# Kernel optimization log

Measured on AMD Instinct MI355X. Metric: run time of the kernel, lower is better.

## Reference

```python
import jax, jax.numpy as jnp
import numpy as np

N_A = 50000   # 'user' nodes
N_B = 50000   # 'item' nodes
E = 1000000   # edges per relation
IN, HID, OUT = 128, 128, 64


def setup_inputs() -> dict:
    key = jax.random.key(0)
    ks = jax.random.split(key, 24)
    def glorot(k, shape):
        scale = 1.0 / np.sqrt(shape[0])
        return jax.random.normal(k, shape, jnp.float32) * scale
    inp = {
        "feat_A": jax.random.normal(ks[0], (N_A, IN), jnp.float32),
        "feat_B": jax.random.normal(ks[1], (N_B, IN), jnp.float32),
        "rates_src": jax.random.randint(ks[2], (E,), 0, N_A, jnp.int32),
        "rates_dst": jax.random.randint(ks[3], (E,), 0, N_B, jnp.int32),
        "ratedby_src": jax.random.randint(ks[4], (E,), 0, N_B, jnp.int32),
        "ratedby_dst": jax.random.randint(ks[5], (E,), 0, N_A, jnp.int32),
        "follows_src": jax.random.randint(ks[6], (E,), 0, N_A, jnp.int32),
        "follows_dst": jax.random.randint(ks[7], (E,), 0, N_A, jnp.int32),
        "neg_src": jax.random.randint(ks[8], (E,), 0, N_A, jnp.int32),
        "neg_dst": jax.random.randint(ks[9], (E,), 0, N_B, jnp.int32),
        "W1_rates": glorot(ks[10], (IN, HID)),   "b1_rates": jnp.zeros((HID,), jnp.float32),
        "W1_ratedby": glorot(ks[11], (IN, HID)), "b1_ratedby": jnp.zeros((HID,), jnp.float32),
        "W1_follows": glorot(ks[12], (IN, HID)), "b1_follows": jnp.zeros((HID,), jnp.float32),
        "W2_rates": glorot(ks[13], (HID, OUT)),   "b2_rates": jnp.zeros((OUT,), jnp.float32),
        "W2_ratedby": glorot(ks[14], (HID, OUT)), "b2_ratedby": jnp.zeros((OUT,), jnp.float32),
        "W2_follows": glorot(ks[15], (HID, OUT)), "b2_follows": jnp.zeros((OUT,), jnp.float32),
    }
    return inp


def _graph_conv(x_src, W, b, src, dst, n_src, n_dst):
    # DGL GraphConv, norm='both': D_dst^{-1/2} A D_src^{-1/2} (X W) + b
    ones = jnp.ones(src.shape[0], x_src.dtype)
    deg_out = jnp.maximum(jax.ops.segment_sum(ones, src, num_segments=n_src), 1.0)
    deg_in = jnp.maximum(jax.ops.segment_sum(ones, dst, num_segments=n_dst), 1.0)
    h = (x_src * (deg_out ** -0.5)[:, None]) @ W          # [n_src, d_out]
    agg = jax.ops.segment_sum(h[src], dst, num_segments=n_dst)  # SpMM
    return agg * (deg_in ** -0.5)[:, None] + b


def reference(feat_A, feat_B,
              W1_rates, b1_rates, W1_ratedby, b1_ratedby, W1_follows, b1_follows,
              W2_rates, b2_rates, W2_ratedby, b2_ratedby, W2_follows, b2_follows,
              rates_src, rates_dst, ratedby_src, ratedby_dst,
              follows_src, follows_dst, neg_src, neg_dst):
    # --- RGCN layer 1 (HeteroGraphConv, aggregate='sum') ---
    hB = _graph_conv(feat_A, W1_rates, b1_rates, rates_src, rates_dst, N_A, N_B)
    hA = (_graph_conv(feat_B, W1_ratedby, b1_ratedby, ratedby_src, ratedby_dst, N_B, N_A)
          + _graph_conv(feat_A, W1_follows, b1_follows, follows_src, follows_dst, N_A, N_A))
    hA = jax.nn.relu(hA)
    hB = jax.nn.relu(hB)
    # --- RGCN layer 2 ---
    oB = _graph_conv(hA, W2_rates, b2_rates, rates_src, rates_dst, N_A, N_B)
    oA = (_graph_conv(hB, W2_ratedby, b2_ratedby, ratedby_src, ratedby_dst, N_B, N_A)
          + _graph_conv(hA, W2_follows, b2_follows, follows_src, follows_dst, N_A, N_A))
    # --- HeteroInnerProduct (u_dot_v on etype 'rates') for pos and neg graphs ---
    pos_score = jnp.sum(oA[rates_src] * oB[rates_dst], axis=1, keepdims=True)  # [E, 1]
    neg_score = jnp.sum(oA[neg_src] * oB[neg_dst], axis=1, keepdims=True)      # [E, 1]
    return pos_score, neg_score
```

## Files before the change

### kernel.cpp

```cpp
#include <hip/hip_runtime.h>
#include <hip/hip_fp16.h>
#include <cstddef>
#include <type_traits>

#define N_NODES 50000
#define E_EDGES 1000000
#define NBUCK 196
#define ACHUNK 3907
#define MTILES 3125
#define HB 96
#define HCHUNK 10417
#define GB1 384
#define GB2 256

typedef _Float16 f16x8 __attribute__((ext_vector_type(8)));
typedef float f32x4 __attribute__((ext_vector_type(4)));

__global__ __launch_bounds__(256) void fused0(
        const float* __restrict__ w0, const float* __restrict__ w1,
        const float* __restrict__ w2, const float* __restrict__ w3,
        const float* __restrict__ w4, const float* __restrict__ w5,
        __half* __restrict__ Wt,
        const int* __restrict__ rs, const int* __restrict__ rd,
        const int* __restrict__ bs, const int* __restrict__ bd,
        const int* __restrict__ fs, const int* __restrict__ fd,
        int* __restrict__ bphist) {
    int bx = blockIdx.x;
    if (bx < 6 * HB) {
        __shared__ int l[NBUCK];
        int arr = bx / HB, blk = bx % HB;
        const int* idx = arr == 0 ? rs : arr == 1 ? rd : arr == 2 ? bs
                       : arr == 3 ? bd : arr == 4 ? fs : fd;
        for (int b = threadIdx.x; b < NBUCK; b += 256) l[b] = 0;
        __syncthreads();
        int e0 = blk * HCHUNK;
        int e1 = e0 + HCHUNK; if (e1 > E_EDGES) e1 = E_EDGES;
        for (int i = e0 + threadIdx.x; i < e1; i += 256)
            atomicAdd(&l[((unsigned)idx[i]) >> 8], 1);
        __syncthreads();
        int* dst = bphist + (size_t)(arr * HB + blk) * NBUCK;
        for (int b = threadIdx.x; b < NBUCK; b += 256) dst[b] = l[b];
        return;
    }
    bx -= 6 * HB;
    int m = bx / 16, part = bx % 16;
    const float* W = m == 0 ? w0 : m == 1 ? w1 : m == 2 ? w2 : m == 3 ? w3 : m == 4 ? w4 : w5;
    __half* Tt = Wt + (m < 3 ? m * 16384 : 49152 + (m - 3) * 8192);
    int ncol = m < 3 ? 128 : 64;
    int tot = 128 * ncol;
    for (int i = part * 256 + threadIdx.x; i < tot; i += 16 * 256) {
        int n = i >> 7, k = i & 127;
        Tt[i] = __float2half(W[k * ncol + n]);
    }
}

__global__ void bucket_scan_par(const int* __restrict__ bphist, int* __restrict__ gbase,
                                int* __restrict__ gcur) {
    int arr = blockIdx.x;
    int t = threadIdx.x;
    int c = 0;
    if (t < NBUCK) {
        const int* p = bphist + (size_t)arr * HB * NBUCK + t;
#pragma unroll 8
        for (int blk = 0; blk < HB; blk++) c += p[(size_t)blk * NBUCK];
    }
    int lane = t & 63, wid = t >> 6;
    __shared__ int wsum[4];
    int v = c;
#pragma unroll
    for (int o = 1; o < 64; o <<= 1) { int u = __shfl_up(v, o); if (lane >= o) v += u; }
    if (lane == 63) wsum[wid] = v;
    __syncthreads();
    int base = 0;
    for (int ww = 0; ww < wid; ww++) base += wsum[ww];
    int excl = base + v - c;
    if (t < NBUCK) {
        gbase[arr * (NBUCK + 1) + t] = excl;
        gcur[arr * NBUCK + t] = excl;
    }
    if (t == 255) gbase[arr * (NBUCK + 1) + NBUCK] = base + v;
}

__global__ __launch_bounds__(256) void fused_bin(
        const int* __restrict__ rs, const int* __restrict__ rd,
        const int* __restrict__ bs, const int* __restrict__ bd,
        const int* __restrict__ fs, const int* __restrict__ fd,
        int* __restrict__ gcur, unsigned* __restrict__ pairs,
        unsigned char* __restrict__ sbytes) {
    int y = blockIdx.y;
    __shared__ int lcnt[NBUCK];
    __shared__ int lbase[NBUCK];
    int e0 = blockIdx.x * ACHUNK;
    int e1 = e0 + ACHUNK; if (e1 > E_EDGES) e1 = E_EDGES;
    for (int b = threadIdx.x; b < NBUCK; b += 256) lcnt[b] = 0;
    __syncthreads();
    if (y < 3) {
        int rel = y, arr = 2 * rel + 1;
        const int* src = rel == 0 ? rs : rel == 1 ? bs : fs;
        const int* dst = rel == 0 ? rd : rel == 1 ? bd : fd;
        for (int i = e0 + threadIdx.x; i < e1; i += 256)
            atomicAdd(&lcnt[((unsigned)dst[i]) >> 8], 1);
        __syncthreads();
        for (int b = threadIdx.x; b < NBUCK; b += 256) {
            lbase[b] = lcnt[b] ? atomicAdd(&gcur[arr * NBUCK + b], lcnt[b]) : 0;
            lcnt[b] = 0;
        }
        __syncthreads();
        unsigned* pp = pairs + (size_t)rel * E_EDGES;
        for (int i = e0 + threadIdx.x; i < e1; i += 256) {
            int d = dst[i];
            int b = ((unsigned)d) >> 8;
            int p = lbase[b] + atomicAdd(&lcnt[b], 1);
            pp[p] = ((unsigned)(d & 255) << 16) | (unsigned)src[i];
        }
    } else {
        int rel = y - 3, arr = 2 * rel;
        const int* src = rel == 0 ? rs : rel == 1 ? bs : fs;
        for (int i = e0 + threadIdx.x; i < e1; i += 256)
            atomicAdd(&lcnt[((unsigned)src[i]) >> 8], 1);
        __syncthreads();
        for (int b = threadIdx.x; b < NBUCK; b += 256) {
            lbase[b] = lcnt[b] ? atomicAdd(&gcur[arr * NBUCK + b], lcnt[b]) : 0;
            lcnt[b] = 0;
        }
        __syncthreads();
        unsigned char* sb = sbytes + (size_t)rel * E_EDGES;
        for (int i = e0 + threadIdx.x; i < e1; i += 256) {
            int s = src[i];
            int b = ((unsigned)s) >> 8;
            int p = lbase[b] + atomicAdd(&lcnt[b], 1);
            sb[p] = (unsigned char)(s & 255);
        }
    }
}

__global__ __launch_bounds__(256) void fused_finish(
        const unsigned* __restrict__ pairs, const unsigned char* __restrict__ sbytes,
        const int* __restrict__ gbase, int* __restrict__ row_ptr,
        float* __restrict__ scales, int* __restrict__ col) {
    int y = blockIdx.y, b = blockIdx.x, t = threadIdx.x;
    __shared__ int cnt[256];
    __shared__ int rowbase[256];
    __shared__ int wsum[4];
    if (y < 3) {
        int rel = y, arr = 2 * rel;
        int p0 = gbase[arr * (NBUCK + 1) + b];
        int p1 = gbase[arr * (NBUCK + 1) + b + 1];
        const unsigned char* sb = sbytes + (size_t)rel * E_EDGES;
        cnt[t] = 0;
        __syncthreads();
        for (int i = p0 + t; i < p1; i += 256)
            atomicAdd(&cnt[sb[i]], 1);
        __syncthreads();
        int node = b * 256 + t;
        if (node < N_NODES) {
            int c = cnt[t]; if (c < 1) c = 1;
            scales[(size_t)arr * N_NODES + node] = 1.0f / sqrtf((float)c);
        }
    } else {
        int rel = y - 3, arr = 2 * rel + 1;
        int gb = gbase[arr * (NBUCK + 1) + b];
        int ge = gbase[arr * (NBUCK + 1) + b + 1];
        const unsigned* pp = pairs + (size_t)rel * E_EDGES;
        cnt[t] = 0;
        __syncthreads();
        for (int i = gb + t; i < ge; i += 256)
            atomicAdd(&cnt[pp[i] >> 16], 1);
        __syncthreads();
        int lane = t & 63, wid = t >> 6;
        int c0 = cnt[t];
        int v = c0;
#pragma unroll
        for (int o = 1; o < 64; o <<= 1) { int u = __shfl_up(v, o); if (lane >= o) v += u; }
        if (lane == 63) wsum[wid] = v;
        __syncthreads();
        int base = gb;
        for (int w = 0; w < wid; w++) base += wsum[w];
        int excl = base + v - c0;
        rowbase[t] = excl;
        int node = b * 256 + t;
        if (node <= N_NODES)
            row_ptr[(size_t)rel * (N_NODES + 1) + node] = excl;
        if (node < N_NODES) {
            int c = c0; if (c < 1) c = 1;
            scales[(size_t)arr * N_NODES + node] = 1.0f / sqrtf((float)c);
        }
        cnt[t] = 0;
        __syncthreads();
        int* cl = col + (size_t)rel * E_EDGES;
        for (int i = gb + t; i < ge; i += 256) {
            unsigned p = pp[i];
            int dl = p >> 16;
            int slot = rowbase[dl] + atomicAdd(&cnt[dl], 1);
            cl[slot] = (int)(p & 0xFFFFu);
        }
    }
}

template <int NCOL, typename XT>
__device__ __forceinline__ void gemm_body(const XT* __restrict__ X,
                                          const float* __restrict__ sc,
                                          const __half* __restrict__ Wt,
                                          __half* __restrict__ T,
                                          int bxr, int nblocks) {
    constexpr int NHALF = NCOL / 64;
    int gw = bxr * 4 + ((int)threadIdx.x >> 6);
    int lane = threadIdx.x & 63;
    int half_id = gw % NHALF;
    int mstream = gw / NHALF;
    int nstreams = nblocks * 4 / NHALF;
    int l15 = lane & 15, g = lane >> 4;

    f16x8 b[4][4];
    {
        const __half* wb = Wt + ((size_t)half_id * 64 + l15) * 128 + g * 8;
#pragma unroll
        for (int nt = 0; nt < 4; nt++)
#pragma unroll
            for (int kb = 0; kb < 4; kb++)
                b[nt][kb] = *(const f16x8*)(wb + nt * 16 * 128 + kb * 32);
    }

    for (int mt = mstream; mt < MTILES; mt += nstreams) {
        int m0 = mt * 16;
        f16x8 a[4];
        if constexpr (std::is_same<XT, float>::value) {
            const float* xr = X + (size_t)(m0 + l15) * 128 + g * 8;
#pragma unroll
            for (int kb = 0; kb < 4; kb++) {
                float4 u = *(const float4*)(xr + kb * 32);
                float4 v = *(const float4*)(xr + kb * 32 + 4);
                f16x8 t;
                t[0] = (_Float16)u.x; t[1] = (_Float16)u.y;
                t[2] = (_Float16)u.z; t[3] = (_Float16)u.w;
                t[4] = (_Float16)v.x; t[5] = (_Float16)v.y;
                t[6] = (_Float16)v.z; t[7] = (_Float16)v.w;
                a[kb] = t;
            }
        } else {
            const _Float16* xr = (const _Float16*)X + (size_t)(m0 + l15) * 128 + g * 8;
#pragma unroll
            for (int kb = 0; kb < 4; kb++)
                a[kb] = *(const f16x8*)(xr + kb * 32);
        }
        f32x4 acc[4];
#pragma unroll
        for (int nt = 0; nt < 4; nt++) acc[nt] = (f32x4){0.f, 0.f, 0.f, 0.f};
#pragma unroll
        for (int kb = 0; kb < 4; kb++)
#pragma unroll
            for (int nt = 0; nt < 4; nt++)
                acc[nt] = __builtin_amdgcn_mfma_f32_16x16x32_f16(a[kb], b[nt][kb], acc[nt], 0, 0, 0);
        int mrow = m0 + g * 4;
#pragma unroll
        for (int j = 0; j < 4; j++) {
            float sj = sc[mrow + j];
            __half* tj = T + (size_t)(mrow + j) * NCOL + half_id * 64 + l15;
            tj[0]  = __float2half(acc[0][j] * sj);
            tj[16] = __float2half(acc[1][j] * sj);
            tj[32] = __float2half(acc[2][j] * sj);
            tj[48] = __float2half(acc[3][j] * sj);
        }
    }
}

__global__ __launch_bounds__(256) void gemm_l1(const float* __restrict__ fA,
                                               const float* __restrict__ fB,
                                               const float* __restrict__ scales,
                                               const __half* __restrict__ Wt,
                                               __half* __restrict__ T012) {
    int rel = blockIdx.x / GB1, bxr = blockIdx.x % GB1;
    const float* X = (rel == 1) ? fB : fA;
    const float* sc = scales + (rel == 0 ? 0 : rel == 1 ? 2 * N_NODES : 4 * N_NODES);
    const __half* W = Wt + rel * 16384;
    __half* T = T012 + (size_t)rel * N_NODES * 128;
    gemm_body<128, float>(X, sc, W, T, bxr, GB1);
}

__global__ __launch_bounds__(256) void gemm_l2(const __half* __restrict__ hA,
                                               const __half* __restrict__ hB,
                                               const float* __restrict__ scales,
                                               const __half* __restrict__ Wt,
                                               __half* __restrict__ Tp) {
    int rel = blockIdx.x / GB2, bxr = blockIdx.x % GB2;
    const __half* X = (rel == 1) ? hB : hA;
    const float* sc = scales + (rel == 0 ? 0 : rel == 1 ? 2 * N_NODES : 4 * N_NODES);
    const __half* W = Wt + 49152 + rel * 8192;
    __half* T = Tp + (size_t)rel * N_NODES * 64;
    gemm_body<64, __half>(X, sc, W, T, bxr, GB2);
}

__global__ __launch_bounds__(256) void spmm_l1(
        const int* __restrict__ row_ptr, const int* __restrict__ col,
        const __half* __restrict__ T012, const float* __restrict__ scales,
        const float* __restrict__ b1r, const float* __restrict__ b1rb,
        const float* __restrict__ b1f,
        __half* __restrict__ hB, __half* __restrict__ hA) {
    int w = (blockIdx.x * blockDim.x + threadIdx.x) >> 6;
    int lane = threadIdx.x & 63;
    unsigned loff = (unsigned)lane << 2;
    const char* T0 = (const char*)T012;
    const char* T1 = T0 + (size_t)N_NODES * 256;
    const char* T2 = T1 + (size_t)N_NODES * 256;
#define LDT(B, c) __half22float2(*(const __half2*)((B) + (((unsigned)(c) << 8) + loff)))
    if (w < N_NODES / 2) {
        const int* cl = col;
        int rowA = w * 2, rowB = rowA + 1;
        int eA = row_ptr[rowA], EA = row_ptr[rowA + 1];
        int eB = EA, EB = row_ptr[rowB + 1];
        float axA = 0.f, ayA = 0.f, axB = 0.f, ayB = 0.f;
        while (eA + 4 <= EA && eB + 4 <= EB) {
            int a0 = cl[eA], a1 = cl[eA+1], a2 = cl[eA+2], a3 = cl[eA+3];
            int b0 = cl[eB], b1 = cl[eB+1], b2 = cl[eB+2], b3 = cl[eB+3];
            float2 v0 = LDT(T0, a0), v1 = LDT(T0, a1), v2 = LDT(T0, a2), v3 = LDT(T0, a3);
            float2 u0 = LDT(T0, b0), u1 = LDT(T0, b1), u2 = LDT(T0, b2), u3 = LDT(T0, b3);
            axA += (v0.x + v1.x) + (v2.x + v3.x); ayA += (v0.y + v1.y) + (v2.y + v3.y);
            axB += (u0.x + u1.x) + (u2.x + u3.x); ayB += (u0.y + u1.y) + (u2.y + u3.y);
            eA += 4; eB += 4;
        }
        while (eA + 4 <= EA) {
            int a0 = cl[eA], a1 = cl[eA+1], a2 = cl[eA+2], a3 = cl[eA+3];
            float2 v0 = LDT(T0, a0), v1 = LDT(T0, a1), v2 = LDT(T0, a2), v3 = LDT(T0, a3);
            axA += (v0.x + v1.x) + (v2.x + v3.x); ayA += (v0.y + v1.y) + (v2.y + v3.y);
            eA += 4;
        }
        while (eB + 4 <= EB) {
            int b0 = cl[eB], b1 = cl[eB+1], b2 = cl[eB+2], b3 = cl[eB+3];
            float2 u0 = LDT(T0, b0), u1 = LDT(T0, b1), u2 = LDT(T0, b2), u3 = LDT(T0, b3);
            axB += (u0.x + u1.x) + (u2.x + u3.x); ayB += (u0.y + u1.y) + (u2.y + u3.y);
            eB += 4;
        }
        while (eA < EA && eB < EB) {
            float2 v = LDT(T0, cl[eA]), u = LDT(T0, cl[eB]);
            axA += v.x; ayA += v.y; axB += u.x; ayB += u.y;
            eA++; eB++;
        }
        for (; eA < EA; eA++) { float2 v = LDT(T0, cl[eA]); axA += v.x; ayA += v.y; }
        for (; eB < EB; eB++) { float2 v = LDT(T0, cl[eB]); axB += v.x; ayB += v.y; }
        float bx = b1r[2 * lane], by = b1r[2 * lane + 1];
        float sA = scales[N_NODES + rowA], sB = scales[N_NODES + rowB];
        float ox = fmaxf(fmaf(axA, sA, bx), 0.f), oy = fmaxf(fmaf(ayA, sA, by), 0.f);
        *(__half2*)(hB + (size_t)rowA * 128 + 2 * lane) = __floats2half2_rn(ox, oy);
        ox = fmaxf(fmaf(axB, sB, bx), 0.f); oy = fmaxf(fmaf(ayB, sB, by), 0.f);
        *(__half2*)(hB + (size_t)rowB * 128 + 2 * lane) = __floats2half2_rn(ox, oy);
    } else {
        int r = w - N_NODES / 2;
        const int* rp1 = row_ptr + (N_NODES + 1);
        const int* rp2 = row_ptr + 2 * (N_NODES + 1);
        const int* cl1 = col + E_EDGES;
        const int* cl2 = col + 2 * (size_t)E_EDGES;
        int e1 = rp1[r], E1 = rp1[r + 1];
        int e2 = rp2[r], E2 = rp2[r + 1];
        float a1x = 0.f, a1y = 0.f, a2x = 0.f, a2y = 0.f;
        while (e1 + 4 <= E1 && e2 + 4 <= E2) {
            int a0 = cl1[e1], a1 = cl1[e1+1], a2 = cl1[e1+2], a3 = cl1[e1+3];
            int b0 = cl2[e2], b1 = cl2[e2+1], b2 = cl2[e2+2], b3 = cl2[e2+3];
            float2 v0 = LDT(T1, a0), v1 = LDT(T1, a1), v2 = LDT(T1, a2), v3 = LDT(T1, a3);
            float2 u0 = LDT(T2, b0), u1 = LDT(T2, b1), u2 = LDT(T2, b2), u3 = LDT(T2, b3);
            a1x += (v0.x + v1.x) + (v2.x + v3.x); a1y += (v0.y + v1.y) + (v2.y + v3.y);
            a2x += (u0.x + u1.x) + (u2.x + u3.x); a2y += (u0.y + u1.y) + (u2.y + u3.y);
            e1 += 4; e2 += 4;
        }
        while (e1 + 4 <= E1) {
            int a0 = cl1[e1], a1 = cl1[e1+1], a2 = cl1[e1+2], a3 = cl1[e1+3];
            float2 v0 = LDT(T1, a0), v1 = LDT(T1, a1), v2 = LDT(T1, a2), v3 = LDT(T1, a3);
            a1x += (v0.x + v1.x) + (v2.x + v3.x); a1y += (v0.y + v1.y) + (v2.y + v3.y);
            e1 += 4;
        }
        while (e2 + 4 <= E2) {
            int b0 = cl2[e2], b1 = cl2[e2+1], b2 = cl2[e2+2], b3 = cl2[e2+3];
            float2 u0 = LDT(T2, b0), u1 = LDT(T2, b1), u2 = LDT(T2, b2), u3 = LDT(T2, b3);
            a2x += (u0.x + u1.x) + (u2.x + u3.x); a2y += (u0.y + u1.y) + (u2.y + u3.y);
            e2 += 4;
        }
        while (e1 < E1 && e2 < E2) {
            float2 v = LDT(T1, cl1[e1]), u = LDT(T2, cl2[e2]);
            a1x += v.x; a1y += v.y; a2x += u.x; a2y += u.y;
            e1++; e2++;
        }
        for (; e1 < E1; e1++) { float2 v = LDT(T1, cl1[e1]); a1x += v.x; a1y += v.y; }
        for (; e2 < E2; e2++) { float2 v = LDT(T2, cl2[e2]); a2x += v.x; a2y += v.y; }
        float s1 = scales[3 * N_NODES + r], s2 = scales[5 * N_NODES + r];
        float ox = a1x * s1 + a2x * s2 + b1rb[2 * lane] + b1f[2 * lane];
        float oy = a1y * s1 + a2y * s2 + b1rb[2 * lane + 1] + b1f[2 * lane + 1];
        ox = fmaxf(ox, 0.f); oy = fmaxf(oy, 0.f);
        *(__half2*)(hA + (size_t)r * 128 + 2 * lane) = __floats2half2_rn(ox, oy);
    }
#undef LDT
}

__global__ __launch_bounds__(256) void spmm_l2(
        const int* __restrict__ row_ptr, const int* __restrict__ col,
        const __half* __restrict__ Tp, const float* __restrict__ scales,
        const float* __restrict__ b2r, const float* __restrict__ b2rb,
        const float* __restrict__ b2f,
        __half* __restrict__ oB, __half* __restrict__ oA) {
    int g = (blockIdx.x * blockDim.x + threadIdx.x) >> 5;
    int l2 = threadIdx.x & 31;
    unsigned loff = (unsigned)l2 << 2;
    const char* T0 = (const char*)Tp;
    const char* T1 = T0 + (size_t)N_NODES * 128;
    const char* T2 = T1 + (size_t)N_NODES * 128;
#define LDT(B, c) __half22float2(*(const __half2*)((B) + (((unsigned)(c) << 7) + loff)))
    if (g < N_NODES / 2) {
        const int* cl = col;
        int rowA = g * 2, rowB = rowA + 1;
        int eA = row_ptr[rowA], EA = row_ptr[rowA + 1];
        int eB = EA, EB = row_ptr[rowB + 1];
        float axA = 0.f, ayA = 0.f, axB = 0.f, ayB = 0.f;
        while (eA + 4 <= EA && eB + 4 <= EB) {
            int a0 = cl[eA], a1 = cl[eA+1], a2 = cl[eA+2], a3 = cl[eA+3];
            int b0 = cl[eB], b1 = cl[eB+1], b2 = cl[eB+2], b3 = cl[eB+3];
            float2 v0 = LDT(T0, a0), v1 = LDT(T0, a1), v2 = LDT(T0, a2), v3 = LDT(T0, a3);
            float2 u0 = LDT(T0, b0), u1 = LDT(T0, b1), u2 = LDT(T0, b2), u3 = LDT(T0, b3);
            axA += (v0.x + v1.x) + (v2.x + v3.x); ayA += (v0.y + v1.y) + (v2.y + v3.y);
            axB += (u0.x + u1.x) + (u2.x + u3.x); ayB += (u0.y + u1.y) + (u2.y + u3.y);
            eA += 4; eB += 4;
        }
        while (eA + 4 <= EA) {
            int a0 = cl[eA], a1 = cl[eA+1], a2 = cl[eA+2], a3 = cl[eA+3];
            float2 v0 = LDT(T0, a0), v1 = LDT(T0, a1), v2 = LDT(T0, a2), v3 = LDT(T0, a3);
            axA += (v0.x + v1.x) + (v2.x + v3.x); ayA += (v0.y + v1.y) + (v2.y + v3.y);
            eA += 4;
        }
        while (eB + 4 <= EB) {
            int b0 = cl[eB], b1 = cl[eB+1], b2 = cl[eB+2], b3 = cl[eB+3];
            float2 u0 = LDT(T0, b0), u1 = LDT(T0, b1), u2 = LDT(T0, b2), u3 = LDT(T0, b3);
            axB += (u0.x + u1.x) + (u2.x + u3.x); ayB += (u0.y + u1.y) + (u2.y + u3.y);
            eB += 4;
        }
        while (eA < EA && eB < EB) {
            float2 v = LDT(T0, cl[eA]), u = LDT(T0, cl[eB]);
            axA += v.x; ayA += v.y; axB += u.x; ayB += u.y;
            eA++; eB++;
        }
        for (; eA < EA; eA++) { float2 v = LDT(T0, cl[eA]); axA += v.x; ayA += v.y; }
        for (; eB < EB; eB++) { float2 v = LDT(T0, cl[eB]); axB += v.x; ayB += v.y; }
        float bx = b2r[2 * l2], by = b2r[2 * l2 + 1];
        float sA = scales[N_NODES + rowA], sB = scales[N_NODES + rowB];
        *(__half2*)(oB + (size_t)rowA * 64 + 2 * l2) =
            __floats2half2_rn(fmaf(axA, sA, bx), fmaf(ayA, sA, by));
        *(__half2*)(oB + (size_t)rowB * 64 + 2 * l2) =
            __floats2half2_rn(fmaf(axB, sB, bx), fmaf(ayB, sB, by));
    } else {
        int r = g - N_NODES / 2;
        const int* rp1 = row_ptr + (N_NODES + 1);
        const int* rp2 = row_ptr + 2 * (N_NODES + 1);
        const int* cl1 = col + E_EDGES;
        const int* cl2 = col + 2 * (size_t)E_EDGES;
        int e1 = rp1[r], E1 = rp1[r + 1];
        int e2 = rp2[r], E2 = rp2[r + 1];
        float a1x = 0.f, a1y = 0.f, a2x = 0.f, a2y = 0.f;
        while (e1 + 4 <= E1 && e2 + 4 <= E2) {
            int a0 = cl1[e1], a1 = cl1[e1+1], a2 = cl1[e1+2], a3 = cl1[e1+3];
            int b0 = cl2[e2], b1 = cl2[e2+1], b2 = cl2[e2+2], b3 = cl2[e2+3];
            float2 v0 = LDT(T1, a0), v1 = LDT(T1, a1), v2 = LDT(T1, a2), v3 = LDT(T1, a3);
            float2 u0 = LDT(T2, b0), u1 = LDT(T2, b1), u2 = LDT(T2, b2), u3 = LDT(T2, b3);
            a1x += (v0.x + v1.x) + (v2.x + v3.x); a1y += (v0.y + v1.y) + (v2.y + v3.y);
            a2x += (u0.x + u1.x) + (u2.x + u3.x); a2y += (u0.y + u1.y) + (u2.y + u3.y);
            e1 += 4; e2 += 4;
        }
        while (e1 + 4 <= E1) {
            int a0 = cl1[e1], a1 = cl1[e1+1], a2 = cl1[e1+2], a3 = cl1[e1+3];
            float2 v0 = LDT(T1, a0), v1 = LDT(T1, a1), v2 = LDT(T1, a2), v3 = LDT(T1, a3);
            a1x += (v0.x + v1.x) + (v2.x + v3.x); a1y += (v0.y + v1.y) + (v2.y + v3.y);
            e1 += 4;
        }
        while (e2 + 4 <= E2) {
            int b0 = cl2[e2], b1 = cl2[e2+1], b2 = cl2[e2+2], b3 = cl2[e2+3];
            float2 u0 = LDT(T2, b0), u1 = LDT(T2, b1), u2 = LDT(T2, b2), u3 = LDT(T2, b3);
            a2x += (u0.x + u1.x) + (u2.x + u3.x); a2y += (u0.y + u1.y) + (u2.y + u3.y);
            e2 += 4;
        }
        while (e1 < E1 && e2 < E2) {
            float2 v = LDT(T1, cl1[e1]), u = LDT(T2, cl2[e2]);
            a1x += v.x; a1y += v.y; a2x += u.x; a2y += u.y;
            e1++; e2++;
        }
        for (; e1 < E1; e1++) { float2 v = LDT(T1, cl1[e1]); a1x += v.x; a1y += v.y; }
        for (; e2 < E2; e2++) { float2 v = LDT(T2, cl2[e2]); a2x += v.x; a2y += v.y; }
        float s1 = scales[3 * N_NODES + r], s2 = scales[5 * N_NODES + r];
        float ox = a1x * s1 + a2x * s2 + b2rb[2 * l2] + b2f[2 * l2];
        float oy = a1y * s1 + a2y * s2 + b2rb[2 * l2 + 1] + b2f[2 * l2 + 1];
        *(__half2*)(oA + (size_t)r * 64 + 2 * l2) = __floats2half2_rn(ox, oy);
    }
#undef LDT
}

__global__ __launch_bounds__(256) void score2(const __half* __restrict__ oA,
                                              const __half* __restrict__ oB,
                                              const int* __restrict__ ps,
                                              const int* __restrict__ pd,
                                              const int* __restrict__ ns,
                                              const int* __restrict__ nd,
                                              float* __restrict__ out) {
    int g = (blockIdx.x * blockDim.x + threadIdx.x) >> 4;
    int l = threadIdx.x & 15;
    int ng = (gridDim.x * blockDim.x) >> 4;
    const char* A = (const char*)oA;
    const char* B = (const char*)oB;
    unsigned loff = (unsigned)l << 3;
#define SCORE_LOOP(SRC, DST, OUT)                                               \
    for (int e0 = g * 2; e0 < E_EDGES; e0 += ng * 2) {                          \
        int e1 = e0 + 1;                                                        \
        int s0 = SRC[e0], d0 = DST[e0], s1 = SRC[e1], d1 = DST[e1];             \
        union { uint2 u; __half2 h[2]; } a0, b0, a1, b1;                        \
        a0.u = *(const uint2*)(A + (((unsigned)s0 << 7) + loff));               \
        b0.u = *(const uint2*)(B + (((unsigned)d0 << 7) + loff));               \
        a1.u = *(const uint2*)(A + (((unsigned)s1 << 7) + loff));               \
        b1.u = *(const uint2*)(B + (((unsigned)d1 << 7) + loff));               \
        float2 fa, fb;                                                          \
        fa = __half22float2(a0.h[0]); fb = __half22float2(b0.h[0]);             \
        float p0 = fa.x * fb.x + fa.y * fb.y;                                   \
        fa = __half22float2(a0.h[1]); fb = __half22float2(b0.h[1]);             \
        p0 += fa.x * fb.x + fa.y * fb.y;                                        \
        fa = __half22float2(a1.h[0]); fb = __half22float2(b1.h[0]);             \
        float p1 = fa.x * fb.x + fa.y * fb.y;                                   \
        fa = __half22float2(a1.h[1]); fb = __half22float2(b1.h[1]);             \
        p1 += fa.x * fb.x + fa.y * fb.y;                                        \
        p0 += __shfl_xor(p0, 8); p1 += __shfl_xor(p1, 8);                       \
        p0 += __shfl_xor(p0, 4); p1 += __shfl_xor(p1, 4);                       \
        p0 += __shfl_xor(p0, 2); p1 += __shfl_xor(p1, 2);                       \
        p0 += __shfl_xor(p0, 1); p1 += __shfl_xor(p1, 1);                       \
        if (l == 0) { OUT[e0] = p0; OUT[e1] = p1; }                             \
    }
    SCORE_LOOP(ps, pd, out)
    float* outn = out + E_EDGES;
    SCORE_LOOP(ns, nd, outn)
#undef SCORE_LOOP
}

extern "C" void kernel_launch(void* const* d_in, const int* in_sizes, int n_in,
                              void* d_out, int out_size, void* d_ws, size_t ws_size,
                              hipStream_t stream) {
    const float* feat_A     = (const float*)d_in[0];
    const float* feat_B     = (const float*)d_in[1];
    const int* rates_src    = (const int*)d_in[2];
    const int* rates_dst    = (const int*)d_in[3];
    const int* ratedby_src  = (const int*)d_in[4];
    const int* ratedby_dst  = (const int*)d_in[5];
    const int* follows_src  = (const int*)d_in[6];
    const int* follows_dst  = (const int*)d_in[7];
    const int* neg_src      = (const int*)d_in[8];
    const int* neg_dst      = (const int*)d_in[9];
    const float* W1_rates   = (const float*)d_in[10];
    const float* b1_rates   = (const float*)d_in[11];
    const float* W1_ratedby = (const float*)d_in[12];
    const float* b1_ratedby = (const float*)d_in[13];
    const float* W1_follows = (const float*)d_in[14];
    const float* b1_follows = (const float*)d_in[15];
    const float* W2_rates   = (const float*)d_in[16];
    const float* b2_rates   = (const float*)d_in[17];
    const float* W2_ratedby = (const float*)d_in[18];
    const float* b2_ratedby = (const float*)d_in[19];
    const float* W2_follows = (const float*)d_in[20];
    const float* b2_follows = (const float*)d_in[21];

    const int N = N_NODES, E = E_EDGES;

    char* ws = (char*)d_ws;
    size_t off = 0;
    auto alloc = [&](size_t bytes) -> void* {
        void* p = ws + off;
        off += (bytes + 255) & ~(size_t)255;
        return p;
    };
    float* scales = (float*)alloc((size_t)6 * N * 4);
    int* row_ptr  = (int*)alloc((size_t)3 * (N + 1) * 4);
    int* bphist   = (int*)alloc((size_t)6 * HB * NBUCK * 4);
    int* gbase    = (int*)alloc((size_t)6 * (NBUCK + 1) * 4);
    int* gcur     = (int*)alloc((size_t)6 * NBUCK * 4);
    int* col      = (int*)alloc((size_t)3 * E * 4);
    unsigned* pairs = (unsigned*)alloc((size_t)3 * E * 4);
    unsigned char* sbytes = (unsigned char*)alloc((size_t)3 * E);
    __half* T012  = (__half*)alloc((size_t)3 * N * 128 * 2);
    __half* Tp    = (__half*)alloc((size_t)3 * N * 64 * 2);
    __half* hA    = (__half*)alloc((size_t)N * 128 * 2);
    __half* hB    = (__half*)alloc((size_t)N * 128 * 2);
    __half* oA    = (__half*)alloc((size_t)N * 64 * 2);
    __half* oB    = (__half*)alloc((size_t)N * 64 * 2);
    __half* Wt    = (__half*)alloc((size_t)(3 * 128 * 128 + 3 * 128 * 64) * 2);
    (void)ws_size;

    fused0<<<6 * HB + 96, 256, 0, stream>>>(W1_rates, W1_ratedby, W1_follows,
                                            W2_rates, W2_ratedby, W2_follows, Wt,
                                            rates_src, rates_dst, ratedby_src,
                                            ratedby_dst, follows_src, follows_dst,
                                            bphist);
    bucket_scan_par<<<6, 256, 0, stream>>>(bphist, gbase, gcur);
    fused_bin<<<dim3(256, 6), 256, 0, stream>>>(rates_src, rates_dst, ratedby_src,
                                                ratedby_dst, follows_src, follows_dst,
                                                gcur, pairs, sbytes);
    fused_finish<<<dim3(NBUCK, 6), 256, 0, stream>>>(pairs, sbytes, gbase,
                                                     row_ptr, scales, col);

    gemm_l1<<<3 * GB1, 256, 0, stream>>>(feat_A, feat_B, scales, Wt, T012);
    spmm_l1<<<(3 * N / 2) / 4, 256, 0, stream>>>(row_ptr, col, T012, scales,
                                                 b1_rates, b1_ratedby, b1_follows,
                                                 hB, hA);
    gemm_l2<<<3 * GB2, 256, 0, stream>>>(hA, hB, scales, Wt, Tp);
    spmm_l2<<<(3 * N / 2) / 8, 256, 0, stream>>>(row_ptr, col, Tp, scales,
                                                 b2_rates, b2_ratedby, b2_follows,
                                                 oB, oA);
    score2<<<8192, 256, 0, stream>>>(oA, oB, rates_src, rates_dst,
                                     neg_src, neg_dst, (float*)d_out);
}
```

Measured before the change: 358.9 us.

## Slice transformed features column-wise so SpMM gathers stay L2-resident per slice

The GEMM epilogue now writes the transformed features in a column-sliced layout: 8 slices of 16 (layer 1) or 8 (layer 2) halfs per node, each slice stored contiguously. Both SpMM kernels are rewritten so each block handles one column slice, and blocks are interleaved across slices. Within a wave, sub-groups split a row's edges, and the partial sums are combined with shuffles. The goal is a smaller gather working set per slice, so random neighbour loads hit cache more often. The cost is re-reading the CSR indices once per slice, predicated padding rounds, and narrower 4-byte scattered stores in the GEMM epilogue.

```diff
diff --git a/kernel.cpp b/kernel.cpp
--- a/kernel.cpp
+++ b/kernel.cpp
@@ -12,6 +12,7 @@
 #define HCHUNK 10417
 #define GB1 384
 #define GB2 256
+#define SLNB 1024
 
 typedef _Float16 f16x8 __attribute__((ext_vector_type(8)));
 typedef float f32x4 __attribute__((ext_vector_type(4)));
@@ -255,11 +256,16 @@
 #pragma unroll
         for (int j = 0; j < 4; j++) {
             float sj = sc[mrow + j];
-            __half* tj = T + (size_t)(mrow + j) * NCOL + half_id * 64 + l15;
-            tj[0]  = __float2half(acc[0][j] * sj);
-            tj[16] = __float2half(acc[1][j] * sj);
-            tj[32] = __float2half(acc[2][j] * sj);
-            tj[48] = __float2half(acc[3][j] * sj);
+#pragma unroll
+            for (int nt = 0; nt < 4; nt++) {
+                int colv = half_id * 64 + nt * 16 + l15;
+                __half val = __float2half(acc[nt][j] * sj);
+                if constexpr (NCOL == 128) {
+                    T[((size_t)(colv >> 4) * N_NODES + mrow + j) * 16 + (colv & 15)] = val;
+                } else {
+                    T[((size_t)(colv >> 3) * N_NODES + mrow + j) * 8 + (colv & 7)] = val;
+                }
+            }
         }
     }
 }
@@ -296,97 +302,83 @@
         const float* __restrict__ b1r, const float* __restrict__ b1rb,
         const float* __restrict__ b1f,
         __half* __restrict__ hB, __half* __restrict__ hA) {
-    int w = (blockIdx.x * blockDim.x + threadIdx.x) >> 6;
+    int slice = blockIdx.x & 7;
+    int wslice = (blockIdx.x >> 3) * 4 + ((int)threadIdx.x >> 6);
+    const int nws = SLNB * 4;
     int lane = threadIdx.x & 63;
-    unsigned loff = (unsigned)lane << 2;
-    const char* T0 = (const char*)T012;
-    const char* T1 = T0 + (size_t)N_NODES * 256;
-    const char* T2 = T1 + (size_t)N_NODES * 256;
-#define LDT(B, c) __half22float2(*(const __half2*)((B) + (((unsigned)(c) << 8) + loff)))
-    if (w < N_NODES / 2) {
-        const int* cl = col;
-        int rowA = w * 2, rowB = rowA + 1;
-        int eA = row_ptr[rowA], EA = row_ptr[rowA + 1];
-        int eB = EA, EB = row_ptr[rowB + 1];
-        float axA = 0.f, ayA = 0.f, axB = 0.f, ayB = 0.f;
-        while (eA + 4 <= EA && eB + 4 <= EB) {
-            int a0 = cl[eA], a1 = cl[eA+1], a2 = cl[eA+2], a3 = cl[eA+3];
-            int b0 = cl[eB], b1 = cl[eB+1], b2 = cl[eB+2], b3 = cl[eB+3];
-            float2 v0 = LDT(T0, a0), v1 = LDT(T0, a1), v2 = LDT(T0, a2), v3 = LDT(T0, a3);
-            float2 u0 = LDT(T0, b0), u1 = LDT(T0, b1), u2 = LDT(T0, b2), u3 = LDT(T0, b3);
-            axA += (v0.x + v1.x) + (v2.x + v3.x); ayA += (v0.y + v1.y) + (v2.y + v3.y);
-            axB += (u0.x + u1.x) + (u2.x + u3.x); ayB += (u0.y + u1.y) + (u2.y + u3.y);
-            eA += 4; eB += 4;
-        }
-        while (eA + 4 <= EA) {
-            int a0 = cl[eA], a1 = cl[eA+1], a2 = cl[eA+2], a3 = cl[eA+3];
-            float2 v0 = LDT(T0, a0), v1 = LDT(T0, a1), v2 = LDT(T0, a2), v3 = LDT(T0, a3);
-            axA += (v0.x + v1.x) + (v2.x + v3.x); ayA += (v0.y + v1.y) + (v2.y + v3.y);
-            eA += 4;
-        }
-        while (eB + 4 <= EB) {
-            int b0 = cl[eB], b1 = cl[eB+1], b2 = cl[eB+2], b3 = cl[eB+3];
-            float2 u0 = LDT(T0, b0), u1 = LDT(T0, b1), u2 = LDT(T0, b2), u3 = LDT(T0, b3);
-            axB += (u0.x + u1.x) + (u2.x + u3.x); ayB += (u0.y + u1.y) + (u2.y + u3.y);
-            eB += 4;
-        }
-        while (eA < EA && eB < EB) {
-            float2 v = LDT(T0, cl[eA]), u = LDT(T0, cl[eB]);
-            axA += v.x; ayA += v.y; axB += u.x; ayB += u.y;
-            eA++; eB++;
-        }
-        for (; eA < EA; eA++) { float2 v = LDT(T0, cl[eA]); axA += v.x; ayA += v.y; }
-        for (; eB < EB; eB++) { float2 v = LDT(T0, cl[eB]); axB += v.x; ayB += v.y; }
-        float bx = b1r[2 * lane], by = b1r[2 * lane + 1];
-        float sA = scales[N_NODES + rowA], sB = scales[N_NODES + rowB];
-        float ox = fmaxf(fmaf(axA, sA, bx), 0.f), oy = fmaxf(fmaf(ayA, sA, by), 0.f);
-        *(__half2*)(hB + (size_t)rowA * 128 + 2 * lane) = __floats2half2_rn(ox, oy);
-        ox = fmaxf(fmaf(axB, sB, bx), 0.f); oy = fmaxf(fmaf(ayB, sB, by), 0.f);
-        *(__half2*)(hB + (size_t)rowB * 128 + 2 * lane) = __floats2half2_rn(ox, oy);
-    } else {
-        int r = w - N_NODES / 2;
-        const int* rp1 = row_ptr + (N_NODES + 1);
-        const int* rp2 = row_ptr + 2 * (N_NODES + 1);
-        const int* cl1 = col + E_EDGES;
-        const int* cl2 = col + 2 * (size_t)E_EDGES;
-        int e1 = rp1[r], E1 = rp1[r + 1];
-        int e2 = rp2[r], E2 = rp2[r + 1];
-        float a1x = 0.f, a1y = 0.f, a2x = 0.f, a2y = 0.f;
-        while (e1 + 4 <= E1 && e2 + 4 <= E2) {
-            int a0 = cl1[e1], a1 = cl1[e1+1], a2 = cl1[e1+2], a3 = cl1[e1+3];
-            int b0 = cl2[e2], b1 = cl2[e2+1], b2 = cl2[e2+2], b3 = cl2[e2+3];
-            float2 v0 = LDT(T1, a0), v1 = LDT(T1, a1), v2 = LDT(T1, a2), v3 = LDT(T1, a3);
-            float2 u0 = LDT(T2, b0), u1 = LDT(T2, b1), u2 = LDT(T2, b2), u3 = LDT(T2, b3);
-            a1x += (v0.x + v1.x) + (v2.x + v3.x); a1y += (v0.y + v1.y) + (v2.y + v3.y);
-            a2x += (u0.x + u1.x) + (u2.x + u3.x); a2y += (u0.y + u1.y) + (u2.y + u3.y);
-            e1 += 4; e2 += 4;
-        }
-        while (e1 + 4 <= E1) {
-            int a0 = cl1[e1], a1 = cl1[e1+1], a2 = cl1[e1+2], a3 = cl1[e1+3];
-            float2 v0 = LDT(T1, a0), v1 = LDT(T1, a1), v2 = LDT(T1, a2), v3 = LDT(T1, a3);
-            a1x += (v0.x + v1.x) + (v2.x + v3.x); a1y += (v0.y + v1.y) + (v2.y + v3.y);
-            e1 += 4;
-        }
-        while (e2 + 4 <= E2) {
-            int b0 = cl2[e2], b1 = cl2[e2+1], b2 = cl2[e2+2], b3 = cl2[e2+3];
-            float2 u0 = LDT(T2, b0), u1 = LDT(T2, b1), u2 = LDT(T2, b2), u3 = LDT(T2, b3);
-            a2x += (u0.x + u1.x) + (u2.x + u3.x); a2y += (u0.y + u1.y) + (u2.y + u3.y);
-            e2 += 4;
-        }
-        while (e1 < E1 && e2 < E2) {
-            float2 v = LDT(T1, cl1[e1]), u = LDT(T2, cl2[e2]);
-            a1x += v.x; a1y += v.y; a2x += u.x; a2y += u.y;
-            e1++; e2++;
-        }
-        for (; e1 < E1; e1++) { float2 v = LDT(T1, cl1[e1]); a1x += v.x; a1y += v.y; }
-        for (; e2 < E2; e2++) { float2 v = LDT(T2, cl2[e2]); a2x += v.x; a2y += v.y; }
-        float s1 = scales[3 * N_NODES + r], s2 = scales[5 * N_NODES + r];
-        float ox = a1x * s1 + a2x * s2 + b1rb[2 * lane] + b1f[2 * lane];
-        float oy = a1y * s1 + a2y * s2 + b1rb[2 * lane + 1] + b1f[2 * lane + 1];
-        ox = fmaxf(ox, 0.f); oy = fmaxf(oy, 0.f);
-        *(__half2*)(hA + (size_t)r * 128 + 2 * lane) = __floats2half2_rn(ox, oy);
-    }
-#undef LDT
+    int stream = lane >> 5;
+    int gi = (lane >> 3) & 3;
+    int li = lane & 7;
+    unsigned lo4 = (unsigned)li << 2;
+    const char* T0 = (const char*)T012 + (size_t)slice * 1600000;
+    const char* T1 = (const char*)T012 + (size_t)(8 + slice) * 1600000;
+    const char* T2 = (const char*)T012 + (size_t)(16 + slice) * 1600000;
+    const int* rp1 = row_ptr + (N_NODES + 1);
+    const int* rp2 = row_ptr + 2 * (N_NODES + 1);
+    const int* cl1 = col + E_EDGES;
+    const int* cl2 = col + 2 * (size_t)E_EDGES;
+    int bi = slice * 16 + 2 * li;
+
+    for (int t = wslice; t < 75000; t += nws) {
+        float ax = 0.f, ay = 0.f;
+        if (t < 25000) {
+            int rowA = t * 2, rowB = rowA + 1;
+            int begA = row_ptr[rowA], EA = row_ptr[rowA + 1], EB = row_ptr[rowB + 1];
+            int myEnd = stream ? EB : EA;
+            int e = (stream ? EA : begA) + gi;
+            int rounds = max(EA - begA, EB - EA);
+            rounds = (rounds + 3) >> 2;
+#pragma unroll 2
+            for (int r = 0; r < rounds; r++) {
+                bool v = e < myEnd;
+                int idx = min(e, myEnd - 1); idx = max(idx, 0);
+                int c = col[idx];
+                float2 val = __half22float2(*(const __half2*)(T0 + ((unsigned)c * 32u + lo4)));
+                if (v) { ax += val.x; ay += val.y; }
+                e += 4;
+            }
+            ax += __shfl_xor(ax, 8);  ay += __shfl_xor(ay, 8);
+            ax += __shfl_xor(ax, 16); ay += __shfl_xor(ay, 16);
+            if (gi == 0) {
+                int row = stream ? rowB : rowA;
+                float s = scales[N_NODES + row];
+                float bx = b1r[bi], by = b1r[bi + 1];
+                float ox = fmaxf(fmaf(ax, s, bx), 0.f);
+                float oy = fmaxf(fmaf(ay, s, by), 0.f);
+                *(__half2*)(hB + (size_t)row * 128 + bi) = __floats2half2_rn(ox, oy);
+            }
+        } else {
+            int r0 = t - 25000;
+            int e1b = rp1[r0], E1 = rp1[r0 + 1];
+            int e2b = rp2[r0], E2 = rp2[r0 + 1];
+            int myEnd = stream ? E2 : E1;
+            int e = (stream ? e2b : e1b) + gi;
+            const int* cp = stream ? cl2 : cl1;
+            const char* Tb = stream ? T2 : T1;
+            int rounds = max(E1 - e1b, E2 - e2b);
+            rounds = (rounds + 3) >> 2;
+#pragma unroll 2
+            for (int r = 0; r < rounds; r++) {
+                bool v = e < myEnd;
+                int idx = min(e, myEnd - 1); idx = max(idx, 0);
+                int c = cp[idx];
+                float2 val = __half22float2(*(const __half2*)(Tb + ((unsigned)c * 32u + lo4)));
+                if (v) { ax += val.x; ay += val.y; }
+                e += 4;
+            }
+            ax += __shfl_xor(ax, 8);  ay += __shfl_xor(ay, 8);
+            ax += __shfl_xor(ax, 16); ay += __shfl_xor(ay, 16);
+            float s = scales[(stream ? 5 : 3) * N_NODES + r0];
+            ax *= s; ay *= s;
+            ax += __shfl_xor(ax, 32); ay += __shfl_xor(ay, 32);
+            if (lane < 8) {
+                float bx = b1rb[bi] + b1f[bi];
+                float by = b1rb[bi + 1] + b1f[bi + 1];
+                float ox = fmaxf(ax + bx, 0.f), oy = fmaxf(ay + by, 0.f);
+                *(__half2*)(hA + (size_t)r0 * 128 + bi) = __floats2half2_rn(ox, oy);
+            }
+        }
+    }
 }
 
 __global__ __launch_bounds__(256) void spmm_l2(
@@ -395,96 +387,83 @@
         const float* __restrict__ b2r, const float* __restrict__ b2rb,
         const float* __restrict__ b2f,
         __half* __restrict__ oB, __half* __restrict__ oA) {
-    int g = (blockIdx.x * blockDim.x + threadIdx.x) >> 5;
-    int l2 = threadIdx.x & 31;
-    unsigned loff = (unsigned)l2 << 2;
-    const char* T0 = (const char*)Tp;
-    const char* T1 = T0 + (size_t)N_NODES * 128;
-    const char* T2 = T1 + (size_t)N_NODES * 128;
-#define LDT(B, c) __half22float2(*(const __half2*)((B) + (((unsigned)(c) << 7) + loff)))
-    if (g < N_NODES / 2) {
-        const int* cl = col;
-        int rowA = g * 2, rowB = rowA + 1;
-        int eA = row_ptr[rowA], EA = row_ptr[rowA + 1];
-        int eB = EA, EB = row_ptr[rowB + 1];
-        float axA = 0.f, ayA = 0.f, axB = 0.f, ayB = 0.f;
-        while (eA + 4 <= EA && eB + 4 <= EB) {
-            int a0 = cl[eA], a1 = cl[eA+1], a2 = cl[eA+2], a3 = cl[eA+3];
-            int b0 = cl[eB], b1 = cl[eB+1], b2 = cl[eB+2], b3 = cl[eB+3];
-            float2 v0 = LDT(T0, a0), v1 = LDT(T0, a1), v2 = LDT(T0, a2), v3 = LDT(T0, a3);
-            float2 u0 = LDT(T0, b0), u1 = LDT(T0, b1), u2 = LDT(T0, b2), u3 = LDT(T0, b3);
-            axA += (v0.x + v1.x) + (v2.x + v3.x); ayA += (v0.y + v1.y) + (v2.y + v3.y);
-            axB += (u0.x + u1.x) + (u2.x + u3.x); ayB += (u0.y + u1.y) + (u2.y + u3.y);
-            eA += 4; eB += 4;
-        }
-        while (eA + 4 <= EA) {
-            int a0 = cl[eA], a1 = cl[eA+1], a2 = cl[eA+2], a3 = cl[eA+3];
-            float2 v0 = LDT(T0, a0), v1 = LDT(T0, a1), v2 = LDT(T0, a2), v3 = LDT(T0, a3);
-            axA += (v0.x + v1.x) + (v2.x + v3.x); ayA += (v0.y + v1.y) + (v2.y + v3.y);
-            eA += 4;
-        }
-        while (eB + 4 <= EB) {
-            int b0 = cl[eB], b1 = cl[eB+1], b2 = cl[eB+2], b3 = cl[eB+3];
-            float2 u0 = LDT(T0, b0), u1 = LDT(T0, b1), u2 = LDT(T0, b2), u3 = LDT(T0, b3);
-            axB += (u0.x + u1.x) + (u2.x + u3.x); ayB += (u0.y + u1.y) + (u2.y + u3.y);
-            eB += 4;
-        }
-        while (eA < EA && eB < EB) {
-            float2 v = LDT(T0, cl[eA]), u = LDT(T0, cl[eB]);
-            axA += v.x; ayA += v.y; axB += u.x; ayB += u.y;
-            eA++; eB++;
-        }
-        for (; eA < EA; eA++) { float2 v = LDT(T0, cl[eA]); axA += v.x; ayA += v.y; }
-        for (; eB < EB; eB++) { float2 v = LDT(T0, cl[eB]); axB += v.x; ayB += v.y; }
-        float bx = b2r[2 * l2], by = b2r[2 * l2 + 1];
-        float sA = scales[N_NODES + rowA], sB = scales[N_NODES + rowB];
-        *(__half2*)(oB + (size_t)rowA * 64 + 2 * l2) =
-            __floats2half2_rn(fmaf(axA, sA, bx), fmaf(ayA, sA, by));
-        *(__half2*)(oB + (size_t)rowB * 64 + 2 * l2) =
-            __floats2half2_rn(fmaf(axB, sB, bx), fmaf(ayB, sB, by));
-    } else {
-        int r = g - N_NODES / 2;
-        const int* rp1 = row_ptr + (N_NODES + 1);
-        const int* rp2 = row_ptr + 2 * (N_NODES + 1);
-        const int* cl1 = col + E_EDGES;
-        const int* cl2 = col + 2 * (size_t)E_EDGES;
-        int e1 = rp1[r], E1 = rp1[r + 1];
-        int e2 = rp2[r], E2 = rp2[r + 1];
-        float a1x = 0.f, a1y = 0.f, a2x = 0.f, a2y = 0.f;
-        while (e1 + 4 <= E1 && e2 + 4 <= E2) {
-            int a0 = cl1[e1], a1 = cl1[e1+1], a2 = cl1[e1+2], a3 = cl1[e1+3];
-            int b0 = cl2[e2], b1 = cl2[e2+1], b2 = cl2[e2+2], b3 = cl2[e2+3];
-            float2 v0 = LDT(T1, a0), v1 = LDT(T1, a1), v2 = LDT(T1, a2), v3 = LDT(T1, a3);
-            float2 u0 = LDT(T2, b0), u1 = LDT(T2, b1), u2 = LDT(T2, b2), u3 = LDT(T2, b3);
-            a1x += (v0.x + v1.x) + (v2.x + v3.x); a1y += (v0.y + v1.y) + (v2.y + v3.y);
-            a2x += (u0.x + u1.x) + (u2.x + u3.x); a2y += (u0.y + u1.y) + (u2.y + u3.y);
-            e1 += 4; e2 += 4;
-        }
-        while (e1 + 4 <= E1) {
-            int a0 = cl1[e1], a1 = cl1[e1+1], a2 = cl1[e1+2], a3 = cl1[e1+3];
-            float2 v0 = LDT(T1, a0), v1 = LDT(T1, a1), v2 = LDT(T1, a2), v3 = LDT(T1, a3);
-            a1x += (v0.x + v1.x) + (v2.x + v3.x); a1y += (v0.y + v1.y) + (v2.y + v3.y);
-            e1 += 4;
-        }
-        while (e2 + 4 <= E2) {
-            int b0 = cl2[e2], b1 = cl2[e2+1], b2 = cl2[e2+2], b3 = cl2[e2+3];
-            float2 u0 = LDT(T2, b0), u1 = LDT(T2, b1), u2 = LDT(T2, b2), u3 = LDT(T2, b3);
-            a2x += (u0.x + u1.x) + (u2.x + u3.x); a2y += (u0.y + u1.y) + (u2.y + u3.y);
-            e2 += 4;
-        }
-        while (e1 < E1 && e2 < E2) {
-            float2 v = LDT(T1, cl1[e1]), u = LDT(T2, cl2[e2]);
-            a1x += v.x; a1y += v.y; a2x += u.x; a2y += u.y;
-            e1++; e2++;
-        }
-        for (; e1 < E1; e1++) { float2 v = LDT(T1, cl1[e1]); a1x += v.x; a1y += v.y; }
-        for (; e2 < E2; e2++) { float2 v = LDT(T2, cl2[e2]); a2x += v.x; a2y += v.y; }
-        float s1 = scales[3 * N_NODES + r], s2 = scales[5 * N_NODES + r];
-        float ox = a1x * s1 + a2x * s2 + b2rb[2 * l2] + b2f[2 * l2];
-        float oy = a1y * s1 + a2y * s2 + b2rb[2 * l2 + 1] + b2f[2 * l2 + 1];
-        *(__half2*)(oA + (size_t)r * 64 + 2 * l2) = __floats2half2_rn(ox, oy);
-    }
-#undef LDT
+    int slice = blockIdx.x & 7;
+    int wslice = (blockIdx.x >> 3) * 4 + ((int)threadIdx.x >> 6);
+    const int nws = SLNB * 4;
+    int lane = threadIdx.x & 63;
+    int stream = lane >> 5;
+    int gi = (lane >> 2) & 7;
+    int li = lane & 3;
+    unsigned lo4 = (unsigned)li << 2;
+    const char* T0 = (const char*)Tp + (size_t)slice * 800000;
+    const char* T1 = (const char*)Tp + (size_t)(8 + slice) * 800000;
+    const char* T2 = (const char*)Tp + (size_t)(16 + slice) * 800000;
+    const int* rp1 = row_ptr + (N_NODES + 1);
+    const int* rp2 = row_ptr + 2 * (N_NODES + 1);
+    const int* cl1 = col + E_EDGES;
+    const int* cl2 = col + 2 * (size_t)E_EDGES;
+    int bi = slice * 8 + 2 * li;
+
+    for (int t = wslice; t < 75000; t += nws) {
+        float ax = 0.f, ay = 0.f;
+        if (t < 25000) {
+            int rowA = t * 2, rowB = rowA + 1;
+            int begA = row_ptr[rowA], EA = row_ptr[rowA + 1], EB = row_ptr[rowB + 1];
+            int myEnd = stream ? EB : EA;
+            int e = (stream ? EA : begA) + gi;
+            int rounds = max(EA - begA, EB - EA);
+            rounds = (rounds + 7) >> 3;
+#pragma unroll 2
+            for (int r = 0; r < rounds; r++) {
+                bool v = e < myEnd;
+                int idx = min(e, myEnd - 1); idx = max(idx, 0);
+                int c = col[idx];
+                float2 val = __half22float2(*(const __half2*)(T0 + ((unsigned)c * 16u + lo4)));
+                if (v) { ax += val.x; ay += val.y; }
+                e += 8;
+            }
+            ax += __shfl_xor(ax, 4);  ay += __shfl_xor(ay, 4);
+            ax += __shfl_xor(ax, 8);  ay += __shfl_xor(ay, 8);
+            ax += __shfl_xor(ax, 16); ay += __shfl_xor(ay, 16);
+            if (gi == 0) {
+                int row = stream ? rowB : rowA;
+                float s = scales[N_NODES + row];
+                float bx = b2r[bi], by = b2r[bi + 1];
+                *(__half2*)(oB + (size_t)row * 64 + bi) =
+                    __floats2half2_rn(fmaf(ax, s, bx), fmaf(ay, s, by));
+            }
+        } else {
+            int r0 = t - 25000;
+            int e1b = rp1[r0], E1 = rp1[r0 + 1];
+            int e2b = rp2[r0], E2 = rp2[r0 + 1];
+            int myEnd = stream ? E2 : E1;
+            int e = (stream ? e2b : e1b) + gi;
+            const int* cp = stream ? cl2 : cl1;
+            const char* Tb = stream ? T2 : T1;
+            int rounds = max(E1 - e1b, E2 - e2b);
+            rounds = (rounds + 7) >> 3;
+#pragma unroll 2
+            for (int r = 0; r < rounds; r++) {
+                bool v = e < myEnd;
+                int idx = min(e, myEnd - 1); idx = max(idx, 0);
+                int c = cp[idx];
+                float2 val = __half22float2(*(const __half2*)(Tb + ((unsigned)c * 16u + lo4)));
+                if (v) { ax += val.x; ay += val.y; }
+                e += 8;
+            }
+            ax += __shfl_xor(ax, 4);  ay += __shfl_xor(ay, 4);
+            ax += __shfl_xor(ax, 8);  ay += __shfl_xor(ay, 8);
+            ax += __shfl_xor(ax, 16); ay += __shfl_xor(ay, 16);
+            float s = scales[(stream ? 5 : 3) * N_NODES + r0];
+            ax *= s; ay *= s;
+            ax += __shfl_xor(ax, 32); ay += __shfl_xor(ay, 32);
+            if (lane < 4) {
+                float bx = b2rb[bi] + b2f[bi];
+                float by = b2rb[bi + 1] + b2f[bi + 1];
+                *(__half2*)(oA + (size_t)r0 * 64 + bi) = __floats2half2_rn(ax + bx, ay + by);
+            }
+        }
+    }
 }
 
 __global__ __launch_bounds__(256) void score2(const __half* __restrict__ oA,
@@ -595,13 +574,13 @@
                                                      row_ptr, scales, col);
 
     gemm_l1<<<3 * GB1, 256, 0, stream>>>(feat_A, feat_B, scales, Wt, T012);
-    spmm_l1<<<(3 * N / 2) / 4, 256, 0, stream>>>(row_ptr, col, T012, scales,
-                                                 b1_rates, b1_ratedby, b1_follows,
-                                                 hB, hA);
+    spmm_l1<<<8 * SLNB, 256, 0, stream>>>(row_ptr, col, T012, scales,
+                                          b1_rates, b1_ratedby, b1_follows,
+                                          hB, hA);
     gemm_l2<<<3 * GB2, 256, 0, stream>>>(hA, hB, scales, Wt, Tp);
-    spmm_l2<<<(3 * N / 2) / 8, 256, 0, stream>>>(row_ptr, col, Tp, scales,
-                                                 b2_rates, b2_ratedby, b2_follows,
-                                                 oB, oA);
+    spmm_l2<<<8 * SLNB, 256, 0, stream>>>(row_ptr, col, Tp, scales,
+                                          b2_rates, b2_ratedby, b2_follows,
+                                          oB, oA);
     score2<<<8192, 256, 0, stream>>>(oA, oB, rates_src, rates_dst,
                                      neg_src, neg_dst, (float*)d_out);
 }
```

Measured after the change: 650.3 us. 81.2% more time.
